# Performance work log

Hardware: AMD Instinct MI355X
Metric: run time of the kernel (lower is better)

The kernel has to match this reference:

```python
import jax, jax.numpy as jnp
import numpy as np

N = 50000      # num nodes
E = 800000     # num edges (avg degree 16)
DIN = 128
DH = 128
DO = 128
BN_EPS = 1e-5


def setup_inputs() -> dict:
    key = jax.random.key(0)
    ks = jax.random.split(key, 16)
    def lin(k, i, o):
        kw, kb = jax.random.split(k)
        s = 1.0 / np.sqrt(i)
        return (jax.random.uniform(kw, (i, o), jnp.float32, -s, s),
                jax.random.uniform(kb, (o,), jnp.float32, -s, s))
    w0_1, b0_1 = lin(ks[0], DIN, DH)
    w0_2, b0_2 = lin(ks[1], DH, DH)
    w1_1, b1_1 = lin(ks[2], DH, DH)
    w1_2, b1_2 = lin(ks[3], DH, DH)
    w2_1, b2_1 = lin(ks[4], DH, DH)
    w2_2, b2_2 = lin(ks[5], DH, DO)
    return {
        "x": jax.random.normal(ks[6], (N, DIN), jnp.float32),
        "edge_index": jax.random.randint(ks[7], (2, E), 0, N, jnp.int64),
        "eps": jnp.zeros((1,), jnp.float32),
        "w0_1": w0_1, "b0_1": b0_1,
        "bn0_g": jnp.ones((DH,), jnp.float32), "bn0_b": jnp.zeros((DH,), jnp.float32),
        "w0_2": w0_2, "b0_2": b0_2,
        "n0_g": jnp.ones((DH,), jnp.float32), "n0_b": jnp.zeros((DH,), jnp.float32),
        "w1_1": w1_1, "b1_1": b1_1, "w1_2": w1_2, "b1_2": b1_2,
        "n1_g": jnp.ones((DH,), jnp.float32), "n1_b": jnp.zeros((DH,), jnp.float32),
        "w2_1": w2_1, "b2_1": b2_1, "w2_2": w2_2, "b2_2": b2_2,
        "n2_g": jnp.ones((DO,), jnp.float32), "n2_b": jnp.zeros((DO,), jnp.float32),
    }


def _bn(h, g, b):
    # BatchNorm1d in training mode: biased batch statistics over nodes
    m = h.mean(0)
    v = jnp.var(h, axis=0)
    return (h - m) * jax.lax.rsqrt(v + BN_EPS) * g + b


def reference(x, edge_index, eps, w0_1, b0_1, bn0_g, bn0_b, w0_2, b0_2, n0_g, n0_b,
              w1_1, b1_1, w1_2, b1_2, n1_g, n1_b,
              w2_1, b2_1, w2_2, b2_2, n2_g, n2_b):
    src, dst = edge_index[0], edge_index[1]

    def agg(h):
        # GIN aggregation: (1+eps)*x_i + sum_{j in N(i)} x_j
        msg = jax.ops.segment_sum(h[src], dst, num_segments=N)
        return (1.0 + eps) * h + msg

    # Layer 0: MLP = Linear -> BN -> ReLU -> Linear, then outer BN + ReLU
    h = agg(x)
    h = h @ w0_1 + b0_1
    h = jax.nn.relu(_bn(h, bn0_g, bn0_b))
    h = h @ w0_2 + b0_2
    h = jax.nn.relu(_bn(h, n0_g, n0_b))

    # Layer 1: MLP = Linear -> ReLU -> Linear, then BN + ReLU
    h = agg(h)
    h = jax.nn.relu(h @ w1_1 + b1_1)
    h = h @ w1_2 + b1_2
    h = jax.nn.relu(_bn(h, n1_g, n1_b))

    # Layer 2: MLP = Linear -> ReLU -> Linear(dim_o), then BN + ReLU
    h = agg(h)
    h = jax.nn.relu(h @ w2_1 + b2_1)
    h = h @ w2_2 + b2_2
    h = jax.nn.relu(_bn(h, n2_g, n2_b))
    return h
```

## Files before the change

kernel.cpp:

```cpp
#include <hip/hip_runtime.h>


typedef __bf16 bf16x8_t __attribute__((ext_vector_type(8)));
typedef float f32x4_t __attribute__((ext_vector_type(4)));
typedef unsigned short u16x8_t __attribute__((ext_vector_type(8)));
typedef unsigned short u16x4_t __attribute__((ext_vector_type(4)));

__device__ __forceinline__ unsigned short f2bf(float f) {
  unsigned u = __builtin_bit_cast(unsigned, f);
  u += 0x7FFFu + ((u >> 16) & 1u);
  return (unsigned short)(u >> 16);
}
__device__ __forceinline__ float bf2f(unsigned short h) {
  unsigned u = ((unsigned)h) << 16;
  return __builtin_bit_cast(float, u);
}

__global__ __launch_bounds__(256) void k_bcount(const int* __restrict__ dst,
                                                unsigned* __restrict__ tot,
                                                int E, int nb) {
  __shared__ unsigned c[256];
  c[threadIdx.x] = 0;
  __syncthreads();
  for (int e = blockIdx.x * 256 + threadIdx.x; e < E; e += gridDim.x * 256)
    atomicAdd(&c[dst[e] >> 8], 1u);
  __syncthreads();
  int t = threadIdx.x;
  if (t < nb && c[t]) atomicAdd(&tot[t], c[t]);
}

__global__ void k_bscan(const unsigned* __restrict__ tot, unsigned* __restrict__ base,
                        unsigned* __restrict__ fill, int nb) {
  __shared__ unsigned s[256];
  int t = threadIdx.x;
  s[t] = (t < nb) ? tot[t] : 0u;
  __syncthreads();
  for (int o = 1; o < 256; o <<= 1) {
    unsigned u = (t >= o) ? s[t - o] : 0u;
    __syncthreads();
    s[t] += u;
    __syncthreads();
  }
  unsigned excl = t ? s[t - 1] : 0u;
  if (t < nb) {
    base[t] = excl;
    fill[t] = excl;
  }
  if (t == nb) base[t] = s[nb - 1];
}

__global__ __launch_bounds__(256) void k_bucket(const int* __restrict__ src,
                                                const int* __restrict__ dst,
                                                unsigned* __restrict__ bucket_fill,
                                                unsigned* __restrict__ ebuf,
                                                int E, int nb, int chunk) {
  __shared__ unsigned cntl[256];
  __shared__ unsigned basel[256];
  __shared__ unsigned fill2[256];
  const int t = threadIdx.x;
  cntl[t] = 0;
  fill2[t] = 0;
  __syncthreads();
  const int lo = blockIdx.x * chunk;
  const int hi = (lo + chunk < E) ? lo + chunk : E;
  for (int e = lo + t; e < hi; e += 256)
    atomicAdd(&cntl[dst[e] >> 8], 1u);
  __syncthreads();
  if (t < nb) basel[t] = atomicAdd(&bucket_fill[t], cntl[t]);
  __syncthreads();
  for (int e = lo + t; e < hi; e += 256) {
    int d = dst[e];
    int b = d >> 8;
    unsigned slot = atomicAdd(&fill2[b], 1u);
    ebuf[basel[b] + slot] = ((unsigned)(d & 255) << 24) | (unsigned)src[e];
  }
}

__global__ __launch_bounds__(256) void k_build(const unsigned* __restrict__ ebuf,
                                               const unsigned* __restrict__ bucket_base,
                                               unsigned* __restrict__ csr_off,
                                               int* __restrict__ csr, int N) {
  __shared__ unsigned cntl[256];
  __shared__ unsigned scl[256];
  __shared__ unsigned startl[256];
  __shared__ unsigned filll[256];
  const int b = blockIdx.x;
  const int t = threadIdx.x;
  const unsigned ebeg = bucket_base[b];
  const unsigned eend = bucket_base[b + 1];
  cntl[t] = 0;
  filll[t] = 0;
  __syncthreads();
  for (unsigned e = ebeg + t; e < eend; e += 256)
    atomicAdd(&cntl[ebuf[e] >> 24], 1u);
  __syncthreads();
  unsigned v = cntl[t];
  scl[t] = v;
  __syncthreads();
  for (int o = 1; o < 256; o <<= 1) {
    unsigned u = (t >= o) ? scl[t - o] : 0u;
    __syncthreads();
    scl[t] += u;
    __syncthreads();
  }
  int node = b * 256 + t;
  if (node < N) csr_off[node] = ebeg + scl[t];
  startl[t] = scl[t] - v;
  __syncthreads();
  for (unsigned e = ebeg + t; e < eend; e += 256) {
    unsigned p = ebuf[e];
    unsigned d = p >> 24;
    unsigned slot = atomicAdd(&filll[d], 1u);
    csr[ebeg + startl[d] + slot] = (int)(p & 0xFFFFFFu);
  }
}

__global__ void k_x2bf(const float* __restrict__ x, unsigned short* __restrict__ xb,
                       int total8) {
  int i = blockIdx.x * 256 + threadIdx.x;
  if (i >= total8) return;
  const float* p = x + (size_t)i * 8;
  float4 f0 = *reinterpret_cast<const float4*>(p);
  float4 f1 = *reinterpret_cast<const float4*>(p + 4);
  u16x8_t o;
  o[0] = f2bf(f0.x); o[1] = f2bf(f0.y); o[2] = f2bf(f0.z); o[3] = f2bf(f0.w);
  o[4] = f2bf(f1.x); o[5] = f2bf(f1.y); o[6] = f2bf(f1.z); o[7] = f2bf(f1.w);
  *reinterpret_cast<u16x8_t*>(xb + (size_t)i * 8) = o;
}

__global__ void k_wt(const float* w0, const float* w1, const float* w2,
                     const float* w3, const float* w4, const float* w5,
                     unsigned short* __restrict__ wT) {
  const float* ws[6] = {w0, w1, w2, w3, w4, w5};
  int m = blockIdx.x >> 4;
  int tl = blockIdx.x & 15;
  int tr = (tl >> 2) * 32;
  int tc = (tl & 3) * 32;
  const float* W = ws[m];
  __shared__ float sm[32][33];
  int r = threadIdx.x >> 3;
  int c4 = (threadIdx.x & 7) * 4;
  float4 v = *reinterpret_cast<const float4*>(&W[(tr + r) * 128 + tc + c4]);
  sm[r][c4 + 0] = v.x; sm[r][c4 + 1] = v.y; sm[r][c4 + 2] = v.z; sm[r][c4 + 3] = v.w;
  __syncthreads();
  u16x4_t o;
  o[0] = f2bf(sm[c4 + 0][r]);
  o[1] = f2bf(sm[c4 + 1][r]);
  o[2] = f2bf(sm[c4 + 2][r]);
  o[3] = f2bf(sm[c4 + 3][r]);
  *reinterpret_cast<u16x4_t*>(&wT[(size_t)m * 16384 + (tc + r) * 128 + tr + c4]) = o;
}

template<int MODE>
__global__ __launch_bounds__(256) void k_agg(
    const unsigned short* __restrict__ Zv, const float* __restrict__ Zself,
    const float* __restrict__ ssum, const float* __restrict__ ssq,
    const float* __restrict__ gg, const float* __restrict__ bb,
    const int* __restrict__ csr, const unsigned* __restrict__ offend,
    const float* __restrict__ epsp, unsigned short* __restrict__ out, int N) {
  __shared__ float scl[128], shl[128];
  const int tid = threadIdx.x;
  if (MODE == 1) {
    if (tid < 128) {
      float inv = 1.f / (float)N;
      float m = ssum[tid] * inv;
      float vv = ssq[tid] * inv - m * m;
      float s = gg[tid] * rsqrtf(vv + 1e-5f);
      scl[tid] = s;
      shl[tid] = bb[tid] - m * s;
    }
    __syncthreads();
  }
  int node = blockIdx.x * 4 + (tid >> 6);
  if (node >= N) return;
  const int lane = tid & 63;
  const int sub = lane >> 4;
  const int t = lane & 15;
  const int c0 = t * 8;

  float sc[8], sh[8];
  if (MODE == 1) {
#pragma unroll
    for (int j = 0; j < 8; ++j) { sc[j] = scl[c0 + j]; sh[j] = shl[c0 + j]; }
  }

  float s[8];
#pragma unroll
  for (int j = 0; j < 8; ++j) s[j] = 0.f;

  auto accum = [&](int row) {
    u16x8_t v = *reinterpret_cast<const u16x8_t*>(Zv + (size_t)row * 128 + c0);
    if (MODE == 0) {
#pragma unroll
      for (int j = 0; j < 8; ++j) s[j] += bf2f(v[j]);
    } else {
#pragma unroll
      for (int j = 0; j < 8; ++j) s[j] += fmaxf(bf2f(v[j]) * sc[j] + sh[j], 0.f);
    }
  };

  const unsigned beg = node ? offend[node - 1] : 0u;
  const unsigned end = offend[node];
  const int deg = (int)(end - beg);
  const int deg64 = deg < 64 ? deg : 64;

  int idx = (lane < deg64) ? csr[beg + lane] : 0;

  const int nIter = (deg64 + 3) >> 2;
  int p = sub;
  int i = 0;
  for (; i + 2 <= nIter; i += 2, p += 8) {
    int r0 = __shfl(idx, p);
    int r1 = __shfl(idx, p + 4);
    if (p < deg64) accum(r0);
    if (p + 4 < deg64) accum(r1);
  }
  if (i < nIter) {
    int r0 = __shfl(idx, p);
    if (p < deg64) accum(r0);
  }

  for (int e = 64 + sub; e < deg; e += 4) accum(csr[beg + e]);

  if (sub == 0) {
    float ep = 1.f + epsp[0];
    if (MODE == 0) {
      const float* Z = Zself + (size_t)node * 128 + c0;
      float4 f0 = *reinterpret_cast<const float4*>(Z);
      float4 f1 = *reinterpret_cast<const float4*>(Z + 4);
      s[0] += ep * f0.x; s[1] += ep * f0.y; s[2] += ep * f0.z; s[3] += ep * f0.w;
      s[4] += ep * f1.x; s[5] += ep * f1.y; s[6] += ep * f1.z; s[7] += ep * f1.w;
    } else {
      u16x8_t v = *reinterpret_cast<const u16x8_t*>(Zv + (size_t)node * 128 + c0);
#pragma unroll
      for (int j = 0; j < 8; ++j)
        s[j] += ep * fmaxf(bf2f(v[j]) * sc[j] + sh[j], 0.f);
    }
  }

#pragma unroll
  for (int j = 0; j < 8; ++j) {
    s[j] += __shfl_xor(s[j], 16);
    s[j] += __shfl_xor(s[j], 32);
  }

  if (sub == 0) {
    u16x8_t o;
#pragma unroll
    for (int j = 0; j < 8; ++j) o[j] = f2bf(s[j]);
    *reinterpret_cast<u16x8_t*>(out + (size_t)node * 128 + c0) = o;
  }
}

template<bool IN_BN, bool OUT_RELU, bool STATS>
__global__ __launch_bounds__(256) void k_mm(
    const unsigned short* __restrict__ A,
    const float* __restrict__ ssum, const float* __restrict__ ssq,
    const float* __restrict__ gg, const float* __restrict__ bb,
    const unsigned short* __restrict__ BT, const float* __restrict__ bias,
    unsigned short* __restrict__ Y, float* __restrict__ osum, float* __restrict__ osq,
    int M, int N) {
  __shared__ __attribute__((aligned(16))) unsigned short Bl[128][136];
  __shared__ float cs[128], cq[128];
  __shared__ float scl[128], shl[128];
  const int tid = threadIdx.x;
  const int r0 = blockIdx.x * 128;
  const int trow = tid >> 4;
  const int tch = (tid & 15) * 8;

#pragma unroll
  for (int pass = 0; pass < 8; ++pass) {
    int n = pass * 16 + trow;
    u16x8_t v = *reinterpret_cast<const u16x8_t*>(&BT[(size_t)n * 128 + tch]);
    *reinterpret_cast<u16x8_t*>(&Bl[n][tch]) = v;
  }
  if (IN_BN && tid < 128) {
    float inv = 1.f / (float)N;
    float m = ssum[tid] * inv;
    float vv = ssq[tid] * inv - m * m;
    float s = gg[tid] * rsqrtf(vv + 1e-5f);
    scl[tid] = s;
    shl[tid] = bb[tid] - m * s;
  }
  if (STATS && tid < 128) { cs[tid] = 0.f; cq[tid] = 0.f; }

  const int wave = tid >> 6;
  const int lane = tid & 63;
  const int lr = lane & 15;
  const int lkb = (lane >> 4) * 8;
  const int wr = r0 + wave * 32;

  u16x8_t araw[2][4];
  const u16x8_t zv = {0, 0, 0, 0, 0, 0, 0, 0};
#pragma unroll
  for (int mr = 0; mr < 2; ++mr) {
    int grow = wr + mr * 16 + lr;
    bool ok = grow < M;
    const unsigned short* Ar = A + (size_t)grow * 128 + lkb;
#pragma unroll
    for (int kc = 0; kc < 4; ++kc)
      araw[mr][kc] = ok ? *reinterpret_cast<const u16x8_t*>(Ar + kc * 32) : zv;
  }
  __syncthreads();

  if (IN_BN) {
#pragma unroll
    for (int kc = 0; kc < 4; ++kc) {
      float scv[8], shv[8];
#pragma unroll
      for (int j = 0; j < 8; ++j) {
        int c = kc * 32 + lkb + j;
        scv[j] = scl[c]; shv[j] = shl[c];
      }
#pragma unroll
      for (int mr = 0; mr < 2; ++mr) {
#pragma unroll
        for (int j = 0; j < 8; ++j)
          araw[mr][kc][j] = f2bf(fmaxf(bf2f(araw[mr][kc][j]) * scv[j] + shv[j], 0.f));
      }
    }
  }

  f32x4_t acc[2][8];
  f32x4_t zero = {0.f, 0.f, 0.f, 0.f};
#pragma unroll
  for (int mr = 0; mr < 2; ++mr)
#pragma unroll
    for (int i = 0; i < 8; ++i) acc[mr][i] = zero;

#pragma unroll
  for (int kc = 0; kc < 4; ++kc) {
    bf16x8_t a0 = __builtin_bit_cast(bf16x8_t, araw[0][kc]);
    bf16x8_t a1 = __builtin_bit_cast(bf16x8_t, araw[1][kc]);
#pragma unroll
    for (int nt = 0; nt < 8; ++nt) {
      bf16x8_t bf = __builtin_bit_cast(bf16x8_t,
          *reinterpret_cast<const u16x8_t*>(&Bl[nt * 16 + lr][kc * 32 + lkb]));
      acc[0][nt] = __builtin_amdgcn_mfma_f32_16x16x32_bf16(a0, bf, acc[0][nt], 0, 0, 0);
      acc[1][nt] = __builtin_amdgcn_mfma_f32_16x16x32_bf16(a1, bf, acc[1][nt], 0, 0, 0);
    }
  }

  const int g = lane >> 4;
#pragma unroll
  for (int mr = 0; mr < 2; ++mr) {
#pragma unroll
    for (int nt = 0; nt < 8; ++nt) {
      int col = nt * 16 + lr;
      float bv = bias[col];
      float s4 = 0.f, q4 = 0.f;
#pragma unroll
      for (int j = 0; j < 4; ++j) {
        int gr = wr + mr * 16 + g * 4 + j;
        float v = acc[mr][nt][j] + bv;
        if (OUT_RELU) v = fmaxf(v, 0.f);
        if (gr < M) {
          Y[(size_t)gr * 128 + col] = f2bf(v);
          if (STATS) { s4 += v; q4 += v * v; }
        }
      }
      if (STATS) {
        s4 += __shfl_xor(s4, 16);
        s4 += __shfl_xor(s4, 32);
        q4 += __shfl_xor(q4, 16);
        q4 += __shfl_xor(q4, 32);
        if (lane < 16) { atomicAdd(&cs[col], s4); atomicAdd(&cq[col], q4); }
      }
    }
  }
  if (STATS) {
    __syncthreads();
    if (tid < 128) {
      atomicAdd(&osum[tid], cs[tid]);
      atomicAdd(&osq[tid], cq[tid]);
    }
  }
}

__global__ __launch_bounds__(256) void k_mm2x(
    const unsigned short* __restrict__ A,
    const unsigned short* __restrict__ BT1, const float* __restrict__ bias1,
    const unsigned short* __restrict__ BT2, const float* __restrict__ bias2,
    unsigned short* __restrict__ Y, float* __restrict__ osum, float* __restrict__ osq,
    int M) {
  __shared__ __attribute__((aligned(16))) unsigned short Al[128][136];
  __shared__ __attribute__((aligned(16))) unsigned short Bl[128][136];
  __shared__ float cs[128], cq[128];
  const int tid = threadIdx.x;
  const int r0 = blockIdx.x * 128;
  const int trow = tid >> 4;
  const int tch = (tid & 15) * 8;

#pragma unroll
  for (int pass = 0; pass < 8; ++pass) {
    int n = pass * 16 + trow;
    u16x8_t v = *reinterpret_cast<const u16x8_t*>(&BT1[(size_t)n * 128 + tch]);
    *reinterpret_cast<u16x8_t*>(&Bl[n][tch]) = v;
  }
  if (tid < 128) { cs[tid] = 0.f; cq[tid] = 0.f; }

  const int wave = tid >> 6;
  const int lane = tid & 63;
  const int lr = lane & 15;
  const int lkb = (lane >> 4) * 8;
  const int wr = r0 + wave * 32;
  const int g = lane >> 4;

  u16x8_t araw[2][4];
  const u16x8_t zv = {0, 0, 0, 0, 0, 0, 0, 0};
#pragma unroll
  for (int mr = 0; mr < 2; ++mr) {
    int grow = wr + mr * 16 + lr;
    bool ok = grow < M;
    const unsigned short* Ar = A + (size_t)grow * 128 + lkb;
#pragma unroll
    for (int kc = 0; kc < 4; ++kc)
      araw[mr][kc] = ok ? *reinterpret_cast<const u16x8_t*>(Ar + kc * 32) : zv;
  }
  __syncthreads();

  f32x4_t acc[2][8];
  f32x4_t zero = {0.f, 0.f, 0.f, 0.f};
#pragma unroll
  for (int mr = 0; mr < 2; ++mr)
#pragma unroll
    for (int i = 0; i < 8; ++i) acc[mr][i] = zero;

#pragma unroll
  for (int kc = 0; kc < 4; ++kc) {
    bf16x8_t a0 = __builtin_bit_cast(bf16x8_t, araw[0][kc]);
    bf16x8_t a1 = __builtin_bit_cast(bf16x8_t, araw[1][kc]);
#pragma unroll
    for (int nt = 0; nt < 8; ++nt) {
      bf16x8_t bf = __builtin_bit_cast(bf16x8_t,
          *reinterpret_cast<const u16x8_t*>(&Bl[nt * 16 + lr][kc * 32 + lkb]));
      acc[0][nt] = __builtin_amdgcn_mfma_f32_16x16x32_bf16(a0, bf, acc[0][nt], 0, 0, 0);
      acc[1][nt] = __builtin_amdgcn_mfma_f32_16x16x32_bf16(a1, bf, acc[1][nt], 0, 0, 0);
    }
  }
  __syncthreads();

#pragma unroll
  for (int pass = 0; pass < 8; ++pass) {
    int n = pass * 16 + trow;
    u16x8_t v = *reinterpret_cast<const u16x8_t*>(&BT2[(size_t)n * 128 + tch]);
    *reinterpret_cast<u16x8_t*>(&Bl[n][tch]) = v;
  }
#pragma unroll
  for (int mr = 0; mr < 2; ++mr) {
#pragma unroll
    for (int nt = 0; nt < 8; ++nt) {
      int col = nt * 16 + lr;
      float bv = bias1[col];
#pragma unroll
      for (int j = 0; j < 4; ++j) {
        Al[wave * 32 + mr * 16 + g * 4 + j][col] = f2bf(fmaxf(acc[mr][nt][j] + bv, 0.f));
      }
    }
  }
  __syncthreads();

#pragma unroll
  for (int mr = 0; mr < 2; ++mr)
#pragma unroll
    for (int i = 0; i < 8; ++i) acc[mr][i] = zero;
#pragma unroll
  for (int kc = 0; kc < 4; ++kc) {
    bf16x8_t a0 = __builtin_bit_cast(bf16x8_t,
        *reinterpret_cast<const u16x8_t*>(&Al[wave * 32 + lr][kc * 32 + lkb]));
    bf16x8_t a1 = __builtin_bit_cast(bf16x8_t,
        *reinterpret_cast<const u16x8_t*>(&Al[wave * 32 + 16 + lr][kc * 32 + lkb]));
#pragma unroll
    for (int nt = 0; nt < 8; ++nt) {
      bf16x8_t bf = __builtin_bit_cast(bf16x8_t,
          *reinterpret_cast<const u16x8_t*>(&Bl[nt * 16 + lr][kc * 32 + lkb]));
      acc[0][nt] = __builtin_amdgcn_mfma_f32_16x16x32_bf16(a0, bf, acc[0][nt], 0, 0, 0);
      acc[1][nt] = __builtin_amdgcn_mfma_f32_16x16x32_bf16(a1, bf, acc[1][nt], 0, 0, 0);
    }
  }

#pragma unroll
  for (int mr = 0; mr < 2; ++mr) {
#pragma unroll
    for (int nt = 0; nt < 8; ++nt) {
      int col = nt * 16 + lr;
      float bv = bias2[col];
      float s4 = 0.f, q4 = 0.f;
#pragma unroll
      for (int j = 0; j < 4; ++j) {
        int gr = wr + mr * 16 + g * 4 + j;
        float v = acc[mr][nt][j] + bv;
        if (gr < M) {
          Y[(size_t)gr * 128 + col] = f2bf(v);
          s4 += v; q4 += v * v;
        }
      }
      s4 += __shfl_xor(s4, 16);
      s4 += __shfl_xor(s4, 32);
      q4 += __shfl_xor(q4, 16);
      q4 += __shfl_xor(q4, 32);
      if (lane < 16) { atomicAdd(&cs[col], s4); atomicAdd(&cq[col], q4); }
    }
  }
  __syncthreads();
  if (tid < 128) {
    atomicAdd(&osum[tid], cs[tid]);
    atomicAdd(&osq[tid], cq[tid]);
  }
}

__global__ void k_final(const unsigned short* __restrict__ Y,
                        const float* __restrict__ ssum, const float* __restrict__ ssq,
                        const float* __restrict__ gg, const float* __restrict__ bb,
                        float* __restrict__ out, int total8, int N) {
  __shared__ float scl[128], shl[128];
  const int tid = threadIdx.x;
  if (tid < 128) {
    float inv = 1.f / (float)N;
    float m = ssum[tid] * inv;
    float vv = ssq[tid] * inv - m * m;
    float s = gg[tid] * rsqrtf(vv + 1e-5f);
    scl[tid] = s;
    shl[tid] = bb[tid] - m * s;
  }
  __syncthreads();
  int i = blockIdx.x * 256 + tid;
  if (i >= total8) return;
  int base = i * 8;
  int c = base & 127;
  u16x8_t v = *reinterpret_cast<const u16x8_t*>(&Y[base]);
  float4 o0, o1;
  o0.x = fmaxf(bf2f(v[0]) * scl[c + 0] + shl[c + 0], 0.f);
  o0.y = fmaxf(bf2f(v[1]) * scl[c + 1] + shl[c + 1], 0.f);
  o0.z = fmaxf(bf2f(v[2]) * scl[c + 2] + shl[c + 2], 0.f);
  o0.w = fmaxf(bf2f(v[3]) * scl[c + 3] + shl[c + 3], 0.f);
  o1.x = fmaxf(bf2f(v[4]) * scl[c + 4] + shl[c + 4], 0.f);
  o1.y = fmaxf(bf2f(v[5]) * scl[c + 5] + shl[c + 5], 0.f);
  o1.z = fmaxf(bf2f(v[6]) * scl[c + 6] + shl[c + 6], 0.f);
  o1.w = fmaxf(bf2f(v[7]) * scl[c + 7] + shl[c + 7], 0.f);
  *reinterpret_cast<float4*>(&out[base]) = o0;
  *reinterpret_cast<float4*>(&out[base + 4]) = o1;
}

extern "C" void kernel_launch(void* const* d_in, const int* in_sizes, int n_in,
                              void* d_out, int out_size, void* d_ws, size_t ws_size,
                              hipStream_t stream) {
  (void)n_in; (void)out_size; (void)ws_size;
  const float* x = (const float*)d_in[0];
  const int* ei = (const int*)d_in[1];
  const float* eps = (const float*)d_in[2];
  const int N = in_sizes[0] / 128;
  const int E = in_sizes[1] / 2;
  const int* src = ei;
  const int* dst = ei + E;

  char* ws = (char*)d_ws;
  size_t off = 0;
  auto alloc = [&](size_t bytes) -> char* {
    char* p = ws + off;
    off += (bytes + 255) & ~(size_t)255;
    return p;
  };
  unsigned* csr_off = (unsigned*)alloc((size_t)N * 4);
  int* csr_src = (int*)alloc((size_t)E * 4);
  unsigned* bucket_tot = (unsigned*)alloc(256 * 4);
  unsigned* bucket_base = (unsigned*)alloc(257 * 4);
  unsigned* bucket_fill = (unsigned*)alloc(256 * 4);
  float* stats = (float*)alloc(8 * 128 * 4);
  unsigned short* wT = (unsigned short*)alloc(6 * 128 * 128 * 2);
  unsigned short* xb = (unsigned short*)alloc((size_t)N * 128 * 2);
  unsigned short* B1 = (unsigned short*)alloc((size_t)N * 128 * 2);
  unsigned short* B2 = (unsigned short*)alloc((size_t)N * 128 * 2);
  unsigned* ebuf = (unsigned*)B1;

  hipMemsetAsync(bucket_tot, 0, 256 * 4, stream);
  hipMemsetAsync(stats, 0, 8 * 128 * 4, stream);

  const int NBUCK = (N + 255) >> 8;
  const int gA = (N + 3) / 4;
  const int gM = (N + 127) / 128;
  const int gF = ((N * 128 / 8) + 255) / 256;
  const int chunk = (E + 255) / 256;

  k_bcount<<<256, 256, 0, stream>>>(dst, bucket_tot, E, NBUCK);
  k_bscan<<<1, 256, 0, stream>>>(bucket_tot, bucket_base, bucket_fill, NBUCK);
  k_bucket<<<256, 256, 0, stream>>>(src, dst, bucket_fill, ebuf, E, NBUCK, chunk);
  k_build<<<NBUCK, 256, 0, stream>>>(ebuf, bucket_base, csr_off, csr_src, N);
  k_x2bf<<<gF, 256, 0, stream>>>(x, xb, N * 128 / 8);
  k_wt<<<96, 256, 0, stream>>>((const float*)d_in[3], (const float*)d_in[7],
                               (const float*)d_in[11], (const float*)d_in[13],
                               (const float*)d_in[17], (const float*)d_in[19], wT);

  k_agg<0><<<gA, 256, 0, stream>>>(xb, x, nullptr, nullptr, nullptr, nullptr,
                                   csr_src, csr_off, eps, B1, N);
  k_mm<false, false, true><<<gM, 256, 0, stream>>>(B1, nullptr, nullptr, nullptr, nullptr,
      wT + 0 * 16384, (const float*)d_in[4], B2, stats + 0, stats + 128, N, N);
  k_mm<true, false, true><<<gM, 256, 0, stream>>>(B2, stats + 0, stats + 128,
      (const float*)d_in[5], (const float*)d_in[6],
      wT + 1 * 16384, (const float*)d_in[8], B1, stats + 256, stats + 384, N, N);

  k_agg<1><<<gA, 256, 0, stream>>>(B1, nullptr, stats + 256, stats + 384,
                                   (const float*)d_in[9], (const float*)d_in[10],
                                   csr_src, csr_off, eps, B2, N);
  k_mm2x<<<gM, 256, 0, stream>>>(B2, wT + 2 * 16384, (const float*)d_in[12],
      wT + 3 * 16384, (const float*)d_in[14], B1, stats + 512, stats + 640, N);

  k_agg<1><<<gA, 256, 0, stream>>>(B1, nullptr, stats + 512, stats + 640,
                                   (const float*)d_in[15], (const float*)d_in[16],
                                   csr_src, csr_off, eps, B2, N);
  k_mm2x<<<gM, 256, 0, stream>>>(B2, wT + 4 * 16384, (const float*)d_in[18],
      wT + 5 * 16384, (const float*)d_in[20], B1, stats + 768, stats + 896, N);

  k_final<<<gF, 256, 0, stream>>>(B1, stats + 768, stats + 896,
                                  (const float*)d_in[21], (const float*)d_in[22],
                                  (float*)d_out, N * 128 / 8, N);
}
```

Measured before the change: 273.1 us.

## Split GIN aggregation into 32-column slices to shrink gather working set

The aggregation kernel now launches four times as many blocks, each handling a 32-column slice of the feature dimension for four nodes. Each lane loads 4 bf16 values, and eight sub-groups walk the neighbour list in parallel. The goal is a smaller per-slice gather footprint (50000 nodes × 64 B) that stays resident in cache, plus more memory-level parallelism. The cost is reading the CSR indices and offsets four times and issuing narrower 8-byte loads. The stats memset is also folded into the scan kernel, removing one memset call.

```diff
diff --git a/kernel.cpp b/kernel.cpp
--- a/kernel.cpp
+++ b/kernel.cpp
@@ -30,9 +30,10 @@
 }
 
 __global__ void k_bscan(const unsigned* __restrict__ tot, unsigned* __restrict__ base,
-                        unsigned* __restrict__ fill, int nb) {
+                        unsigned* __restrict__ fill, float* __restrict__ stats, int nb) {
   __shared__ unsigned s[256];
   int t = threadIdx.x;
+  for (int i = t; i < 1024; i += 256) stats[i] = 0.f;
   s[t] = (t < nb) ? tot[t] : 0u;
   __syncthreads();
   for (int o = 1; o < 256; o <<= 1) {
@@ -157,45 +158,50 @@
     const float* __restrict__ ssum, const float* __restrict__ ssq,
     const float* __restrict__ gg, const float* __restrict__ bb,
     const int* __restrict__ csr, const unsigned* __restrict__ offend,
-    const float* __restrict__ epsp, unsigned short* __restrict__ out, int N) {
-  __shared__ float scl[128], shl[128];
+    const float* __restrict__ epsp, unsigned short* __restrict__ out,
+    int N, int nodeBlocks) {
+  __shared__ float scl[32], shl[32];
   const int tid = threadIdx.x;
+  const int slice = blockIdx.x / nodeBlocks;
+  const int nb = blockIdx.x - slice * nodeBlocks;
+  const int cbase = slice * 32;
   if (MODE == 1) {
-    if (tid < 128) {
+    if (tid < 32) {
+      int c = cbase + tid;
       float inv = 1.f / (float)N;
-      float m = ssum[tid] * inv;
-      float vv = ssq[tid] * inv - m * m;
-      float s = gg[tid] * rsqrtf(vv + 1e-5f);
+      float m = ssum[c] * inv;
+      float vv = ssq[c] * inv - m * m;
+      float s = gg[c] * rsqrtf(vv + 1e-5f);
       scl[tid] = s;
-      shl[tid] = bb[tid] - m * s;
+      shl[tid] = bb[c] - m * s;
     }
     __syncthreads();
   }
-  int node = blockIdx.x * 4 + (tid >> 6);
+  int node = nb * 4 + (tid >> 6);
   if (node >= N) return;
   const int lane = tid & 63;
-  const int sub = lane >> 4;
-  const int t = lane & 15;
-  const int c0 = t * 8;
-
-  float sc[8], sh[8];
+  const int sub = lane >> 3;
+  const int t = lane & 7;
+  const int c0 = cbase + t * 4;
+
+  float sc[4], sh[4];
   if (MODE == 1) {
 #pragma unroll
-    for (int j = 0; j < 8; ++j) { sc[j] = scl[c0 + j]; sh[j] = shl[c0 + j]; }
-  }
-
-  float s[8];
-#pragma unroll
-  for (int j = 0; j < 8; ++j) s[j] = 0.f;
+    for (int j = 0; j < 4; ++j) { sc[j] = scl[t * 4 + j]; sh[j] = shl[t * 4 + j]; }
+  }
+
+  float s[4];
+#pragma unroll
+  for (int j = 0; j < 4; ++j) s[j] = 0.f;
 
   auto accum = [&](int row) {
-    u16x8_t v = *reinterpret_cast<const u16x8_t*>(Zv + (size_t)row * 128 + c0);
+    u16x4_t v = *reinterpret_cast<const u16x4_t*>(Zv + (size_t)row * 128 + c0);
     if (MODE == 0) {
 #pragma unroll
-      for (int j = 0; j < 8; ++j) s[j] += bf2f(v[j]);
+      for (int j = 0; j < 4; ++j) s[j] += bf2f(v[j]);
     } else {
 #pragma unroll
-      for (int j = 0; j < 8; ++j) s[j] += fmaxf(bf2f(v[j]) * sc[j] + sh[j], 0.f);
+      for (int j = 0; j < 4; ++j) s[j] += fmaxf(bf2f(v[j]) * sc[j] + sh[j], 0.f);
     }
   };
 
@@ -206,49 +212,47 @@
 
   int idx = (lane < deg64) ? csr[beg + lane] : 0;
 
-  const int nIter = (deg64 + 3) >> 2;
+  const int nIter = (deg64 + 7) >> 3;
   int p = sub;
   int i = 0;
-  for (; i + 2 <= nIter; i += 2, p += 8) {
+  for (; i + 2 <= nIter; i += 2, p += 16) {
     int r0 = __shfl(idx, p);
-    int r1 = __shfl(idx, p + 4);
+    int r1 = __shfl(idx, p + 8);
     if (p < deg64) accum(r0);
-    if (p + 4 < deg64) accum(r1);
+    if (p + 8 < deg64) accum(r1);
   }
   if (i < nIter) {
     int r0 = __shfl(idx, p);
     if (p < deg64) accum(r0);
   }
 
-  for (int e = 64 + sub; e < deg; e += 4) accum(csr[beg + e]);
+  for (int e = 64 + sub; e < deg; e += 8) accum(csr[beg + e]);
 
   if (sub == 0) {
     float ep = 1.f + epsp[0];
     if (MODE == 0) {
-      const float* Z = Zself + (size_t)node * 128 + c0;
-      float4 f0 = *reinterpret_cast<const float4*>(Z);
-      float4 f1 = *reinterpret_cast<const float4*>(Z + 4);
-      s[0] += ep * f0.x; s[1] += ep * f0.y; s[2] += ep * f0.z; s[3] += ep * f0.w;
-      s[4] += ep * f1.x; s[5] += ep * f1.y; s[6] += ep * f1.z; s[7] += ep * f1.w;
+      float4 f = *reinterpret_cast<const float4*>(Zself + (size_t)node * 128 + c0);
+      s[0] += ep * f.x; s[1] += ep * f.y; s[2] += ep * f.z; s[3] += ep * f.w;
     } else {
-      u16x8_t v = *reinterpret_cast<const u16x8_t*>(Zv + (size_t)node * 128 + c0);
-#pragma unroll
-      for (int j = 0; j < 8; ++j)
+      u16x4_t v = *reinterpret_cast<const u16x4_t*>(Zv + (size_t)node * 128 + c0);
+#pragma unroll
+      for (int j = 0; j < 4; ++j)
         s[j] += ep * fmaxf(bf2f(v[j]) * sc[j] + sh[j], 0.f);
     }
   }
 
 #pragma unroll
-  for (int j = 0; j < 8; ++j) {
+  for (int j = 0; j < 4; ++j) {
+    s[j] += __shfl_xor(s[j], 8);
     s[j] += __shfl_xor(s[j], 16);
     s[j] += __shfl_xor(s[j], 32);
   }
 
   if (sub == 0) {
-    u16x8_t o;
-#pragma unroll
-    for (int j = 0; j < 8; ++j) o[j] = f2bf(s[j]);
-    *reinterpret_cast<u16x8_t*>(out + (size_t)node * 128 + c0) = o;
+    u16x4_t o;
+#pragma unroll
+    for (int j = 0; j < 4; ++j) o[j] = f2bf(s[j]);
+    *reinterpret_cast<u16x4_t*>(out + (size_t)node * 128 + c0) = o;
   }
 }
 
@@ -574,16 +578,16 @@
   unsigned* ebuf = (unsigned*)B1;
 
   hipMemsetAsync(bucket_tot, 0, 256 * 4, stream);
-  hipMemsetAsync(stats, 0, 8 * 128 * 4, stream);
 
   const int NBUCK = (N + 255) >> 8;
-  const int gA = (N + 3) / 4;
+  const int nodeBlocks = (N + 3) / 4;
+  const int gA = 4 * nodeBlocks;
   const int gM = (N + 127) / 128;
   const int gF = ((N * 128 / 8) + 255) / 256;
   const int chunk = (E + 255) / 256;
 
   k_bcount<<<256, 256, 0, stream>>>(dst, bucket_tot, E, NBUCK);
-  k_bscan<<<1, 256, 0, stream>>>(bucket_tot, bucket_base, bucket_fill, NBUCK);
+  k_bscan<<<1, 256, 0, stream>>>(bucket_tot, bucket_base, bucket_fill, stats, NBUCK);
   k_bucket<<<256, 256, 0, stream>>>(src, dst, bucket_fill, ebuf, E, NBUCK, chunk);
   k_build<<<NBUCK, 256, 0, stream>>>(ebuf, bucket_base, csr_off, csr_src, N);
   k_x2bf<<<gF, 256, 0, stream>>>(x, xb, N * 128 / 8);
@@ -592,7 +596,7 @@
                                (const float*)d_in[17], (const float*)d_in[19], wT);
 
   k_agg<0><<<gA, 256, 0, stream>>>(xb, x, nullptr, nullptr, nullptr, nullptr,
-                                   csr_src, csr_off, eps, B1, N);
+                                   csr_src, csr_off, eps, B1, N, nodeBlocks);
   k_mm<false, false, true><<<gM, 256, 0, stream>>>(B1, nullptr, nullptr, nullptr, nullptr,
       wT + 0 * 16384, (const float*)d_in[4], B2, stats + 0, stats + 128, N, N);
   k_mm<true, false, true><<<gM, 256, 0, stream>>>(B2, stats + 0, stats + 128,
@@ -601,13 +605,13 @@
 
   k_agg<1><<<gA, 256, 0, stream>>>(B1, nullptr, stats + 256, stats + 384,
                                    (const float*)d_in[9], (const float*)d_in[10],
-                                   csr_src, csr_off, eps, B2, N);
+                                   csr_src, csr_off, eps, B2, N, nodeBlocks);
   k_mm2x<<<gM, 256, 0, stream>>>(B2, wT + 2 * 16384, (const float*)d_in[12],
       wT + 3 * 16384, (const float*)d_in[14], B1, stats + 512, stats + 640, N);
 
   k_agg<1><<<gA, 256, 0, stream>>>(B1, nullptr, stats + 512, stats + 640,
                                    (const float*)d_in[15], (const float*)d_in[16],
-                                   csr_src, csr_off, eps, B2, N);
+                                   csr_src, csr_off, eps, B2, N, nodeBlocks);
   k_mm2x<<<gM, 256, 0, stream>>>(B2, wT + 4 * 16384, (const float*)d_in[18],
       wT + 5 * 16384, (const float*)d_in[20], B1, stats + 768, stats + 896, N);
 
```

New measurement: 404.9 us. 1.48x slower.

## Add column-sliced layer-0 aggregation kernel and fold stats memset into scan

Applied to the files above, without the earlier changes.

Replaces the first-layer aggregation with a new kernel that splits the 128 feature columns into four 32-column slices. Blocks for the same node chunk are interleaved so gathered rows of the bf16 input share cache lines across neighbouring blocks, and each edge reads 8 bytes per thread with a one-step prefetch of the next CSR index. The statistics buffer is now zeroed inside the single-block scan kernel, which removes a separate memset launch. In exchange the CSR offsets and indices are read four times per node, and each edge issues more, smaller loads.

```diff
diff --git a/kernel.cpp b/kernel.cpp
--- a/kernel.cpp
+++ b/kernel.cpp
@@ -30,9 +30,10 @@
 }
 
 __global__ void k_bscan(const unsigned* __restrict__ tot, unsigned* __restrict__ base,
-                        unsigned* __restrict__ fill, int nb) {
+                        unsigned* __restrict__ fill, float* __restrict__ stats, int nb) {
   __shared__ unsigned s[256];
   int t = threadIdx.x;
+  for (int i = t; i < 1024; i += 256) stats[i] = 0.f;
   s[t] = (t < nb) ? tot[t] : 0u;
   __syncthreads();
   for (int o = 1; o < 256; o <<= 1) {
@@ -149,6 +150,50 @@
   o[2] = f2bf(sm[c4 + 2][r]);
   o[3] = f2bf(sm[c4 + 3][r]);
   *reinterpret_cast<u16x4_t*>(&wT[(size_t)m * 16384 + (tc + r) * 128 + tr + c4]) = o;
+}
+
+__global__ __launch_bounds__(256) void k_aggs(
+    const unsigned short* __restrict__ Zv, const float* __restrict__ Zself,
+    const int* __restrict__ csr, const unsigned* __restrict__ offend,
+    const float* __restrict__ epsp, unsigned short* __restrict__ out, int N) {
+  const int b = blockIdx.x;
+  const int r = b & 7;
+  const int slice = r & 3;
+  const int half = r >> 2;
+  const int g = b >> 3;
+  const int chunk = g * 2 + half;
+  const int tid = threadIdx.x;
+  const int wave = tid >> 6;
+  const int lane = tid & 63;
+  const int grp = lane >> 3;
+  const int q = lane & 7;
+  const int c0 = slice * 32 + q * 4;
+  const int node = chunk * 32 + wave * 8 + grp;
+  if (node >= N) return;
+
+  const unsigned beg = node ? offend[node - 1] : 0u;
+  const unsigned end = offend[node];
+  const float ep = 1.f + epsp[0];
+
+  float s0, s1, s2, s3;
+  {
+    float4 f = *reinterpret_cast<const float4*>(Zself + (size_t)node * 128 + c0);
+    s0 = ep * f.x; s1 = ep * f.y; s2 = ep * f.z; s3 = ep * f.w;
+  }
+
+  unsigned e = beg;
+  int row = (e < end) ? csr[e] : 0;
+  while (e < end) {
+    unsigned e2 = e + 1;
+    int row2 = (e2 < end) ? csr[e2] : 0;
+    u16x4_t v = *reinterpret_cast<const u16x4_t*>(Zv + (size_t)row * 128 + c0);
+    s0 += bf2f(v[0]); s1 += bf2f(v[1]); s2 += bf2f(v[2]); s3 += bf2f(v[3]);
+    e = e2; row = row2;
+  }
+
+  u16x4_t o;
+  o[0] = f2bf(s0); o[1] = f2bf(s1); o[2] = f2bf(s2); o[3] = f2bf(s3);
+  *reinterpret_cast<u16x4_t*>(out + (size_t)node * 128 + c0) = o;
 }
 
 template<int MODE>
@@ -574,16 +619,17 @@
   unsigned* ebuf = (unsigned*)B1;
 
   hipMemsetAsync(bucket_tot, 0, 256 * 4, stream);
-  hipMemsetAsync(stats, 0, 8 * 128 * 4, stream);
 
   const int NBUCK = (N + 255) >> 8;
   const int gA = (N + 3) / 4;
+  const int nodeChunks = (N + 31) / 32;
+  const int gAS = ((nodeChunks + 1) / 2) * 8;
   const int gM = (N + 127) / 128;
   const int gF = ((N * 128 / 8) + 255) / 256;
   const int chunk = (E + 255) / 256;
 
   k_bcount<<<256, 256, 0, stream>>>(dst, bucket_tot, E, NBUCK);
-  k_bscan<<<1, 256, 0, stream>>>(bucket_tot, bucket_base, bucket_fill, NBUCK);
+  k_bscan<<<1, 256, 0, stream>>>(bucket_tot, bucket_base, bucket_fill, stats, NBUCK);
   k_bucket<<<256, 256, 0, stream>>>(src, dst, bucket_fill, ebuf, E, NBUCK, chunk);
   k_build<<<NBUCK, 256, 0, stream>>>(ebuf, bucket_base, csr_off, csr_src, N);
   k_x2bf<<<gF, 256, 0, stream>>>(x, xb, N * 128 / 8);
@@ -591,8 +637,7 @@
                                (const float*)d_in[11], (const float*)d_in[13],
                                (const float*)d_in[17], (const float*)d_in[19], wT);
 
-  k_agg<0><<<gA, 256, 0, stream>>>(xb, x, nullptr, nullptr, nullptr, nullptr,
-                                   csr_src, csr_off, eps, B1, N);
+  k_aggs<<<gAS, 256, 0, stream>>>(xb, x, csr_src, csr_off, eps, B1, N);
   k_mm<false, false, true><<<gM, 256, 0, stream>>>(B1, nullptr, nullptr, nullptr, nullptr,
       wT + 0 * 16384, (const float*)d_in[4], B2, stats + 0, stats + 128, N, N);
   k_mm<true, false, true><<<gM, 256, 0, stream>>>(B2, stats + 0, stats + 128,
```

New measurement: 303.0 us. +11.0%, slower.
